# Performance work log

Measured on AMD Instinct MI355X. Metric: run time of the kernel, lower is better.

## Reference

```python
import jax, jax.numpy as jnp
import numpy as np

D_MODEL = 1024
H = 16
T = 1024
B = 8

def setup_inputs() -> dict:
    key = jax.random.key(0)
    k0, k1, k2, k3, k4 = jax.random.split(key, 5)
    return {
        "x": jax.random.normal(k0, (B, T, D_MODEL), dtype=jnp.float32),
        "Wq": jax.random.normal(k1, (D_MODEL, D_MODEL), dtype=jnp.float32),
        "Wk": jax.random.normal(k2, (D_MODEL, D_MODEL), dtype=jnp.float32),
        "Wv": jax.random.normal(k3, (D_MODEL, D_MODEL), dtype=jnp.float32),
        "Wp": jax.random.normal(k4, (D_MODEL, D_MODEL), dtype=jnp.float32),
    }

def reference(x, Wq, Wk, Wv, Wp):
    b, t, d = x.shape
    dh = d // H
    # projections
    q = (x @ Wq).reshape(b, t, H, dh)
    k = (x @ Wk).reshape(b, t, H, dh)
    v = (x @ Wv).reshape(b, t, H, dh)
    # [b, h, t, t] attention scores, scaled by sqrt(d_head)
    scores = jnp.einsum("bqhd,bkhd->bhqk", q, k) / jnp.sqrt(jnp.float32(dh))
    attn = jax.nn.softmax(scores, axis=-1)
    # [b, h, t, dh] -> [b, t, d]
    out = jnp.einsum("bhqk,bkhd->bqhd", attn, v).reshape(b, t, d)
    return out @ Wp
```

## Files before the change

### kernel.cpp

```cpp
#include <hip/hip_runtime.h>
#include <math.h>


typedef unsigned short u16;
typedef unsigned int u32;
typedef __bf16  bf16x8 __attribute__((ext_vector_type(8)));
typedef unsigned short u16x8 __attribute__((ext_vector_type(8)));
typedef unsigned short u16x4 __attribute__((ext_vector_type(4)));
typedef short s16x4 __attribute__((ext_vector_type(4)));
typedef unsigned int u32x2 __attribute__((ext_vector_type(2)));
typedef float f32x4 __attribute__((ext_vector_type(4)));

#define MFMA16(a,b,c) __builtin_amdgcn_mfma_f32_16x16x32_bf16((a),(b),(c),0,0,0)
#define MFMA16K16(a,b,c) __builtin_amdgcn_mfma_f32_16x16x16bf16_1k((a),(b),(c),0,0,0)

static __device__ __forceinline__ u16 f2b(float f){
  unsigned u = __builtin_bit_cast(unsigned, f);
  u += 0x7fffu + ((u >> 16) & 1u);
  return (u16)(u >> 16);
}
static __device__ __forceinline__ float b2f(u16 h){
  unsigned u = ((unsigned)h) << 16;
  return __builtin_bit_cast(float, u);
}
static __device__ __forceinline__ bf16x8 ldsfrag(const u16* p){
  return __builtin_bit_cast(bf16x8, *(const u16x8*)p);
}
static __device__ __forceinline__ u32 packhi(float fa, float fb){
  return __builtin_amdgcn_perm(__builtin_bit_cast(u32, fa),
                               __builtin_bit_cast(u32, fb), 0x07060302u);
}
static __device__ __forceinline__ void gld16(const void* g, void* l){
  __builtin_amdgcn_global_load_lds(
      (const __attribute__((address_space(1))) void*)g,
      (__attribute__((address_space(3))) void*)l, 16, 0, 0);
}


__global__ __launch_bounds__(256) void split_x_kernel(
    const float* __restrict__ x, u16* __restrict__ xh, u16* __restrict__ xl, int n)
{
  int i = (blockIdx.x * 256 + threadIdx.x) * 8;
  if (i >= n) return;
  float4 v0 = *(const float4*)(x + i);
  float4 v1 = *(const float4*)(x + i + 4);
  float vv[8] = {v0.x, v0.y, v0.z, v0.w, v1.x, v1.y, v1.z, v1.w};
  u16x8 hv, lv;
#pragma unroll
  for (int j = 0; j < 8; j++){
    u16 hb = f2b(vv[j]);
    hv[j] = hb;
    lv[j] = f2b(vv[j] - b2f(hb));
  }
  *(u16x8*)(xh + i) = hv;
  *(u16x8*)(xl + i) = lv;
}

__global__ __launch_bounds__(256) void transpose4_kernel(
    const float* __restrict__ Wq, const float* __restrict__ Wk,
    const float* __restrict__ Wv, const float* __restrict__ Wp,
    u16* __restrict__ qh_, u16* __restrict__ ql_,
    u16* __restrict__ kh_, u16* __restrict__ kl_,
    u16* __restrict__ vt_, u16* __restrict__ pt_)
{
  __shared__ float t[32][33];
  const int z = blockIdx.z;
  const float* W = (z == 0) ? Wq : (z == 1) ? Wk : (z == 2) ? Wv : Wp;
  u16* Th = (z == 0) ? qh_ : (z == 1) ? kh_ : (z == 2) ? vt_ : pt_;
  u16* Tl = (z == 0) ? ql_ : (z == 1) ? kl_ : nullptr;
  int n0 = blockIdx.x * 32, k0 = blockIdx.y * 32;
  int tx = threadIdx.x, ty = threadIdx.y;
#pragma unroll
  for (int i = 0; i < 4; i++){
    int k = k0 + ty + i * 8;
    t[ty + i * 8][tx] = W[(size_t)k * 1024 + n0 + tx];
  }
  __syncthreads();
#pragma unroll
  for (int i = 0; i < 4; i++){
    int n = n0 + ty + i * 8;
    float v = t[tx][ty + i * 8];
    u16 h = f2b(v);
    Th[(size_t)n * 1024 + k0 + tx] = h;
    if (Tl) Tl[(size_t)n * 1024 + k0 + tx] = f2b(v - b2f(h));
  }
}

template<int OUTMODE>
__global__ __launch_bounds__(256) void gemm_bt_kernel(
    const u16* __restrict__ A, const u16* __restrict__ Bt, void* __restrict__ Cv,
    int M, int N, int K)
{
  __shared__ __attribute__((aligned(16))) u16 lA[4096], lB[4096];
  const int tid = threadIdx.x, lane = tid & 63, wave = tid >> 6;
  const int quad = lane >> 4, l15 = lane & 15;
  const int row0 = blockIdx.x * 128, col0 = blockIdx.y * 128;
  const int wm = wave >> 1, wn = wave & 1;
  const int sr = lane >> 2, sc = (lane & 3) * 8;
  f32x4 acc[4][4];
#pragma unroll
  for (int mt = 0; mt < 4; mt++)
#pragma unroll
    for (int nt = 0; nt < 4; nt++) acc[mt][nt] = (f32x4)0.0f;

  for (int k0 = 0; k0 < K; k0 += 32){
#pragma unroll
    for (int i = 0; i < 2; i++){
      int c = wave * 2 + i;
      gld16(A  + (size_t)(row0 + c * 16 + sr) * K + k0 + sc, &lA[c * 512]);
      gld16(Bt + (size_t)(col0 + c * 16 + sr) * K + k0 + sc, &lB[c * 512]);
    }
    __syncthreads();
    bf16x8 a[4], b[4];
#pragma unroll
    for (int t = 0; t < 4; t++){
      a[t] = ldsfrag(&lA[(wm * 64 + t * 16 + l15) * 32 + quad * 8]);
      b[t] = ldsfrag(&lB[(wn * 64 + t * 16 + l15) * 32 + quad * 8]);
    }
#pragma unroll
    for (int mt = 0; mt < 4; mt++)
#pragma unroll
      for (int nt = 0; nt < 4; nt++)
        acc[mt][nt] = MFMA16(a[mt], b[nt], acc[mt][nt]);
    __syncthreads();
  }
  if (OUTMODE == 2){
#pragma unroll
    for (int mt = 0; mt < 4; mt++)
#pragma unroll
      for (int nt = 0; nt < 4; nt++){
        int row = row0 + wm * 64 + mt * 16 + quad * 4;
        int col = col0 + wn * 64 + nt * 16 + l15;
        int bb = row >> 10, tt = row & 1023;
        int hh = (col >> 6) & 15, d = col & 63;
        int bhI = bb * 16 + hh;
        int ktile = tt >> 7, fkt = (tt >> 4) & 7, qF = (tt >> 2) & 3;
        int nd = d >> 4, l15F = d & 15;
        size_t idx = ((((size_t)(bhI * 8 + ktile) * 8 + fkt) * 4 + nd) * 64
                      + qF * 16 + l15F) * 4;
        u16x4 vals;
#pragma unroll
        for (int r = 0; r < 4; r++) vals[r] = f2b(acc[mt][nt][r]);
        *(u16x4*)(((u16*)Cv) + idx) = vals;
      }
  } else {
#pragma unroll
    for (int mt = 0; mt < 4; mt++)
#pragma unroll
      for (int nt = 0; nt < 4; nt++)
#pragma unroll
        for (int r = 0; r < 4; r++){
          int row = row0 + wm * 64 + mt * 16 + quad * 4 + r;
          int col = col0 + wn * 64 + nt * 16 + l15;
          ((float*)Cv)[(size_t)row * N + col] = acc[mt][nt][r];
        }
  }
}

__global__ __launch_bounds__(512, 2) void gemm_qk_kernel(
    const u16* __restrict__ Ah, const u16* __restrict__ Al,
    const u16* __restrict__ Bh, const u16* __restrict__ Bl,
    u16* __restrict__ Qhf, u16* __restrict__ Qlf,
    u16* __restrict__ Khf, u16* __restrict__ Klf, int M, int N, int K)
{
  __shared__ __attribute__((aligned(16))) u16 sA[2][2][8192], sB[2][2][8192];
  const int tid = threadIdx.x, lane = tid & 63, wave = tid >> 6;
  const int quad = lane >> 4, l15 = lane & 15;
  const int wm = wave >> 2, wn = wave & 3;
  const int row0 = blockIdx.x * 256, col0 = blockIdx.y * 256;
  const int f0a = (wave & 3) | ((wave & 4) << 1);
  const int f0b = (wave & 1) | ((wave >> 1) << 2);
  const size_t fstride = (size_t)16 * K;
  const size_t abase = (size_t)(row0 + l15) * K + quad * 8;
  const size_t bbase = (size_t)(col0 + l15) * K + quad * 8;
  (void)M; (void)N;

  f32x4 acc[8][4];
#pragma unroll
  for (int mt = 0; mt < 8; mt++)
#pragma unroll
    for (int nt = 0; nt < 4; nt++) acc[mt][nt] = (f32x4)0.0f;

#define STAGE_ALL(KK, NB) do {                                                           \
    gld16(Ah + abase + (size_t)f0a * fstride + (KK), &sA[NB][0][f0a * 512]);             \
    gld16(Al + abase + (size_t)f0a * fstride + (KK), &sA[NB][1][f0a * 512]);             \
    gld16(Bh + bbase + (size_t)f0b * fstride + (KK), &sB[NB][0][f0b * 512]);             \
    gld16(Bl + bbase + (size_t)f0b * fstride + (KK), &sB[NB][1][f0b * 512]);             \
    gld16(Bh + bbase + (size_t)(f0b + 2) * fstride + (KK), &sB[NB][0][(f0b + 2) * 512]); \
    gld16(Bl + bbase + (size_t)(f0b + 2) * fstride + (KK), &sB[NB][1][(f0b + 2) * 512]); \
    gld16(Ah + abase + (size_t)(f0a + 4) * fstride + (KK), &sA[NB][0][(f0a + 4) * 512]); \
    gld16(Al + abase + (size_t)(f0a + 4) * fstride + (KK), &sA[NB][1][(f0a + 4) * 512]); \
  } while (0)
#define RD_A2(DH, DL, B4, I0, BUF) do {                           \
    _Pragma("unroll")                                             \
    for (int i = (I0); i < (I0) + 2; i++){                        \
      int fa = wm * 8 + (B4) + i;                                 \
      DH[i] = ldsfrag(&sA[BUF][0][fa * 512 + lane * 8]);          \
      DL[i] = ldsfrag(&sA[BUF][1][fa * 512 + lane * 8]);          \
    } } while (0)
#define RD_B2(DH, DL, B2, BUF) do {                               \
    _Pragma("unroll")                                             \
    for (int j = 0; j < 2; j++){                                  \
      int fb = wn * 4 + (B2) + j;                                 \
      DH[j] = ldsfrag(&sB[BUF][0][fb * 512 + lane * 8]);          \
      DL[j] = ldsfrag(&sB[BUF][1][fb * 512 + lane * 8]);          \
    } } while (0)
#define MM(AH, AL, BH, BL, M0, N0) do {                                      \
    __builtin_amdgcn_s_setprio(1);                                           \
    _Pragma("unroll")                                                        \
    for (int i = 0; i < 4; i++)                                              \
      _Pragma("unroll")                                                      \
      for (int j = 0; j < 2; j++){                                           \
        acc[(M0) + i][(N0) + j] = MFMA16(AL[i], BH[j], acc[(M0) + i][(N0) + j]); \
        acc[(M0) + i][(N0) + j] = MFMA16(AH[i], BL[j], acc[(M0) + i][(N0) + j]); \
        acc[(M0) + i][(N0) + j] = MFMA16(AH[i], BH[j], acc[(M0) + i][(N0) + j]); \
      }                                                                      \
    __builtin_amdgcn_s_setprio(0);                                           \
  } while (0)

  const int NT = K >> 5;
  STAGE_ALL(0, 0);

  bf16x8 a0h[4], a0l[4], a1h[4], a1l[4];
  bf16x8 b0h[2], b0l[2], b1h[2], b1l[2];
#pragma unroll 2
  for (int t = 0; t < NT; t++){
    const int buf = t & 1, nb = buf ^ 1;
    const int kn = ((t + 1) & (NT - 1)) * 32;
    asm volatile("s_waitcnt vmcnt(0)" ::: "memory");
    asm volatile("s_barrier" ::: "memory");
    STAGE_ALL(kn, nb);
    RD_A2(a0h, a0l, 0, 0, buf);
    RD_A2(a0h, a0l, 0, 2, buf);
    RD_B2(b0h, b0l, 0, buf);
    RD_B2(b1h, b1l, 2, buf);
    MM(a0h, a0l, b0h, b0l, 0, 0);
    RD_A2(a1h, a1l, 4, 0, buf);
    MM(a0h, a0l, b1h, b1l, 0, 2);
    RD_A2(a1h, a1l, 4, 2, buf);
    RD_B2(b0h, b0l, 0, buf);
    MM(a1h, a1l, b1h, b1l, 4, 2);
    MM(a1h, a1l, b0h, b0l, 4, 0);
  }
  asm volatile("s_waitcnt vmcnt(0)" ::: "memory");

#undef STAGE_ALL
#undef RD_A2
#undef RD_B2
#undef MM

  const bool isQ = (col0 < 1024);
#pragma unroll
  for (int mt = 0; mt < 8; mt++)
#pragma unroll
    for (int nt = 0; nt < 4; nt++)
#pragma unroll
      for (int r = 0; r < 4; r++){
        int row = row0 + wm * 128 + mt * 16 + quad * 4 + r;
        int col = col0 + wn * 64 + nt * 16 + l15;
        int bb = row >> 10, tt = row & 1023;
        int hh = (col >> 6) & 15, d = col & 63;
        int bhI = bb * 16 + hh;
        int kc = d >> 5, qF = (d >> 3) & 3, j = d & 7;
        float v = acc[mt][nt][r];
        u16 hi = f2b(v);
        u16 lo = f2b(v - b2f(hi));
        if (isQ){
          int qtile = tt >> 7, rr = tt & 127;
          int wv = rr >> 5, mtF = (rr >> 4) & 1, l15F = tt & 15;
          size_t idx = ((((size_t)(bhI * 8 + qtile) * 4 + wv) * 2 + mtF) * 2 + kc) * 512
                       + (qF * 16 + l15F) * 8 + j;
          Qhf[idx] = hi; Qlf[idx] = lo;
        } else {
          int ktile = tt >> 7, fkt = (tt >> 4) & 7, l15F = tt & 15;
          size_t idx = (((size_t)(bhI * 8 + ktile) * 8 + fkt) * 2 + kc) * 512
                       + (qF * 16 + l15F) * 8 + j;
          Khf[idx] = hi; Klf[idx] = lo;
        }
      }
}

__global__ __launch_bounds__(256, 3) void attn_kernel(
    const u16* __restrict__ Qhf, const u16* __restrict__ Qlf,
    const u16* __restrict__ Khf, const u16* __restrict__ Klf,
    const u16* __restrict__ Vf, u16* __restrict__ O)
{
  __shared__ __attribute__((aligned(16))) u16 lKh[2][4096], lKl[2][4096], lV[2][4096];
  const int tid = threadIdx.x, lane = tid & 63, wave = tid >> 6;
  const int quad = lane >> 4, l15 = lane & 15;
  const int qt = blockIdx.x >> 7, bh = blockIdx.x & 127;
  const int b = bh >> 4, h = bh & 15;
  const int q0 = qt * 128;
  const float BETA = 0.18033688011112042f;

  bf16x8 qh[2][2], ql[2][2];
  {
    size_t qbase = (size_t)(bh * 8 + qt) * 8192 + wave * 2048 + lane * 8;
    u16* sh = &lKh[0][0];  u16* sl = &lKl[0][0];
#pragma unroll
    for (int i = 0; i < 4; i++){
      gld16(Qhf + qbase + i * 512, sh + wave * 2048 + i * 512);
      gld16(Qlf + qbase + i * 512, sl + wave * 2048 + i * 512);
    }
    __syncthreads();
#pragma unroll
    for (int mt = 0; mt < 2; mt++)
#pragma unroll
      for (int kc = 0; kc < 2; kc++){
        int off = wave * 2048 + (mt * 2 + kc) * 512 + lane * 8;
        qh[mt][kc] = ldsfrag(sh + off);
        ql[mt][kc] = ldsfrag(sl + off);
      }
    __syncthreads();
  }

  float m_i[2] = {-3.0e38f, -3.0e38f}, l_i[2] = {0.0f, 0.0f};
  f32x4 o_acc[2][4];
#pragma unroll
  for (int mt = 0; mt < 2; mt++)
#pragma unroll
    for (int nd = 0; nd < 4; nd++) o_acc[mt][nd] = (f32x4)0.0f;

  const size_t pan = (size_t)bh * 65536;
#pragma unroll
  for (int i = 0; i < 2; i++){
    int c = wave * 2 + i;
    gld16(Khf + pan + c * 512 + lane * 8, &lKh[0][c * 512]);
    gld16(Klf + pan + c * 512 + lane * 8, &lKl[0][c * 512]);
    gld16(Vf  + pan + c * 512 + lane * 8, &lV [0][c * 512]);
  }

#pragma unroll 1
  for (int j = 0; j < 16; j++){
    const int cur = j & 1;
    __syncthreads();
    if (j < 15){
      size_t nb = pan + (size_t)(j + 1) * 4096;
      const int nxt = cur ^ 1;
#pragma unroll
      for (int i = 0; i < 2; i++){
        int c = wave * 2 + i;
        gld16(Khf + nb + c * 512 + lane * 8, &lKh[nxt][c * 512]);
        gld16(Klf + nb + c * 512 + lane * 8, &lKl[nxt][c * 512]);
        gld16(Vf  + nb + c * 512 + lane * 8, &lV [nxt][c * 512]);
      }
    }

    f32x4 s[2][4];
#pragma unroll
    for (int qt2 = 0; qt2 < 2; qt2++)
#pragma unroll
      for (int f4 = 0; f4 < 4; f4++) s[qt2][f4] = (f32x4)0.0f;
#pragma unroll
    for (int f4 = 0; f4 < 4; f4++){
      int aoff = f4 * 1024 + lane * 8;
      bf16x8 kh0 = ldsfrag(&lKh[cur][aoff]);
      bf16x8 kh1 = ldsfrag(&lKh[cur][aoff + 512]);
      bf16x8 kl0 = ldsfrag(&lKl[cur][aoff]);
      bf16x8 kl1 = ldsfrag(&lKl[cur][aoff + 512]);
#pragma unroll
      for (int qt2 = 0; qt2 < 2; qt2++){
        s[qt2][f4] = MFMA16(kl0, qh[qt2][0], s[qt2][f4]);
        s[qt2][f4] = MFMA16(kl1, qh[qt2][1], s[qt2][f4]);
        s[qt2][f4] = MFMA16(kh0, ql[qt2][0], s[qt2][f4]);
        s[qt2][f4] = MFMA16(kh1, ql[qt2][1], s[qt2][f4]);
        s[qt2][f4] = MFMA16(kh0, qh[qt2][0], s[qt2][f4]);
        s[qt2][f4] = MFMA16(kh1, qh[qt2][1], s[qt2][f4]);
      }
    }

    float alpha[2];
#pragma unroll
    for (int qt2 = 0; qt2 < 2; qt2++){
      f32x4 mv = s[qt2][0];
#pragma unroll
      for (int f4 = 1; f4 < 4; f4++){
        mv[0] = fmaxf(mv[0], s[qt2][f4][0]); mv[1] = fmaxf(mv[1], s[qt2][f4][1]);
        mv[2] = fmaxf(mv[2], s[qt2][f4][2]); mv[3] = fmaxf(mv[3], s[qt2][f4][3]);
      }
      float mx = fmaxf(fmaxf(mv[0], mv[1]), fmaxf(mv[2], mv[3]));
      mx = fmaxf(mx, __shfl_xor(mx, 16));
      mx = fmaxf(mx, __shfl_xor(mx, 32));
      float mn = fmaxf(m_i[qt2], mx);
      alpha[qt2] = __builtin_amdgcn_exp2f((m_i[qt2] - mn) * BETA);
      m_i[qt2] = mn;
      float mb = mn * BETA;
      f32x4 ps = (f32x4)0.0f;
#pragma unroll
      for (int f4 = 0; f4 < 4; f4++)
#pragma unroll
        for (int r = 0; r < 4; r++){
          float p = __builtin_amdgcn_exp2f(s[qt2][f4][r] * BETA - mb);
          s[qt2][f4][r] = p;
          ps[r] += p;
        }
      float rs = (ps[0] + ps[1]) + (ps[2] + ps[3]);
      rs += __shfl_xor(rs, 16);
      rs += __shfl_xor(rs, 32);
      l_i[qt2] = l_i[qt2] * alpha[qt2] + rs;
    }

#pragma unroll
    for (int mt = 0; mt < 2; mt++)
#pragma unroll
      for (int r = 0; r < 4; r++){
        float ar = __shfl(alpha[mt], quad * 4 + r);
#pragma unroll
        for (int nd = 0; nd < 4; nd++) o_acc[mt][nd][r] *= ar;
      }

#pragma unroll
    for (int f4 = 0; f4 < 4; f4++){
      s16x4 vb[4];
#pragma unroll
      for (int nd = 0; nd < 4; nd++)
        vb[nd] = __builtin_bit_cast(s16x4,
                   *(const u16x4*)&lV[cur][(f4 * 4 + nd) * 256 + lane * 4]);
#pragma unroll
      for (int qt2 = 0; qt2 < 2; qt2++){
        u32x2 pd;
        pd[0] = packhi(s[qt2][f4][1], s[qt2][f4][0]);
        pd[1] = packhi(s[qt2][f4][3], s[qt2][f4][2]);
        s16x4 pa = __builtin_bit_cast(s16x4, pd);
#pragma unroll
        for (int nd = 0; nd < 4; nd++)
          o_acc[qt2][nd] = MFMA16K16(pa, vb[nd], o_acc[qt2][nd]);
      }
    }
  }

#pragma unroll
  for (int mt = 0; mt < 2; mt++)
#pragma unroll
    for (int r = 0; r < 4; r++){
      float lr = __shfl(l_i[mt], quad * 4 + r);
      float inv = 1.0f / lr;
      int t = q0 + wave * 32 + mt * 16 + quad * 4 + r;
      size_t rowoff = (size_t)(b * 1024 + t) * 1024 + h * 64;
#pragma unroll
      for (int nd = 0; nd < 4; nd++)
        O[rowoff + nd * 16 + l15] = f2b(o_acc[mt][nd][r] * inv);
    }
}

extern "C" void kernel_launch(void* const* d_in, const int* in_sizes, int n_in,
                              void* d_out, int out_size, void* d_ws, size_t ws_size,
                              hipStream_t stream)
{
  const float* x  = (const float*)d_in[0];
  const float* Wq = (const float*)d_in[1];
  const float* Wk = (const float*)d_in[2];
  const float* Wv = (const float*)d_in[3];
  const float* Wp = (const float*)d_in[4];
  float* out = (float*)d_out;
  char* ws = (char*)d_ws;
  const size_t MB = 1024 * 1024;
  u16* xh   = (u16*)(ws + 0);
  u16* xl   = (u16*)(ws + 16 * MB);
  u16* wqkh = (u16*)(ws + 32 * MB);
  u16* wqkl = (u16*)(ws + 36 * MB);
  u16* wvt  = (u16*)(ws + 40 * MB);
  u16* wpt  = (u16*)(ws + 42 * MB);
  u16* Qhf  = (u16*)(ws + 44 * MB);
  u16* Qlf  = (u16*)(ws + 60 * MB);
  u16* Khf  = (u16*)(ws + 76 * MB);
  u16* Klf  = (u16*)(ws + 92 * MB);
  u16* Vf   = (u16*)(ws + 108 * MB);
  u16* obuf = xh;
  (void)in_sizes; (void)n_in; (void)out_size; (void)ws_size;

  split_x_kernel<<<4096, 256, 0, stream>>>(x, xh, xl, 8 * 1024 * 1024);
  transpose4_kernel<<<dim3(32, 32, 4), dim3(32, 8), 0, stream>>>(
      Wq, Wk, Wv, Wp, wqkh, wqkl, wqkh + 1024 * 1024, wqkl + 1024 * 1024, wvt, wpt);
  gemm_qk_kernel<<<dim3(32, 8), 512, 0, stream>>>(xh, xl, wqkh, wqkl,
                                                  Qhf, Qlf, Khf, Klf, 8192, 2048, 1024);
  gemm_bt_kernel<2><<<dim3(64, 8), 256, 0, stream>>>(xh, wvt, (void*)Vf, 8192, 1024, 1024);
  attn_kernel<<<1024, 256, 0, stream>>>(Qhf, Qlf, Khf, Klf, Vf, obuf);
  gemm_bt_kernel<0><<<dim3(64, 8), 256, 0, stream>>>(obuf, wpt, (void*)out, 8192, 1024, 1024);
}
```

Before: 350.7 us.

## Interleave global-to-LDS staging with MFMA phases using extra barriers in QKV GEMM

Splits the per-iteration global-to-LDS prefetch into three groups and issues each between LDS fragment reads and MFMA blocks, with s_barrier after each group. The aim is to spread memory traffic across the compute phases and keep waves in lockstep, in the style of ping-pong scheduling. In exchange it adds four barriers per iteration, which can stall waves if they are not balanced.

```diff
diff --git a/kernel.cpp b/kernel.cpp
--- a/kernel.cpp
+++ b/kernel.cpp
@@ -181,13 +181,17 @@
 #pragma unroll
     for (int nt = 0; nt < 4; nt++) acc[mt][nt] = (f32x4)0.0f;
 
-#define STAGE_ALL(KK, NB) do {                                                           \
-    gld16(Ah + abase + (size_t)f0a * fstride + (KK), &sA[NB][0][f0a * 512]);             \
-    gld16(Al + abase + (size_t)f0a * fstride + (KK), &sA[NB][1][f0a * 512]);             \
-    gld16(Bh + bbase + (size_t)f0b * fstride + (KK), &sB[NB][0][f0b * 512]);             \
-    gld16(Bl + bbase + (size_t)f0b * fstride + (KK), &sB[NB][1][f0b * 512]);             \
+#define STAGE_G0(KK, NB) do {                                              \
+    gld16(Ah + abase + (size_t)f0a * fstride + (KK), &sA[NB][0][f0a * 512]); \
+    gld16(Al + abase + (size_t)f0a * fstride + (KK), &sA[NB][1][f0a * 512]); \
+    gld16(Bh + bbase + (size_t)f0b * fstride + (KK), &sB[NB][0][f0b * 512]); \
+    gld16(Bl + bbase + (size_t)f0b * fstride + (KK), &sB[NB][1][f0b * 512]); \
+  } while (0)
+#define STAGE_G1(KK, NB) do {                                                        \
     gld16(Bh + bbase + (size_t)(f0b + 2) * fstride + (KK), &sB[NB][0][(f0b + 2) * 512]); \
     gld16(Bl + bbase + (size_t)(f0b + 2) * fstride + (KK), &sB[NB][1][(f0b + 2) * 512]); \
+  } while (0)
+#define STAGE_G2(KK, NB) do {                                                        \
     gld16(Ah + abase + (size_t)(f0a + 4) * fstride + (KK), &sA[NB][0][(f0a + 4) * 512]); \
     gld16(Al + abase + (size_t)(f0a + 4) * fstride + (KK), &sA[NB][1][(f0a + 4) * 512]); \
   } while (0)
@@ -217,9 +221,13 @@
       }                                                                      \
     __builtin_amdgcn_s_setprio(0);                                           \
   } while (0)
+#define VMCNT0() asm volatile("s_waitcnt vmcnt(0)" ::: "memory")
+#define BARRIER() asm volatile("s_barrier" ::: "memory")
 
   const int NT = K >> 5;
-  STAGE_ALL(0, 0);
+  STAGE_G0(0, 0);
+  STAGE_G1(0, 0);
+  STAGE_G2(0, 0);
 
   bf16x8 a0h[4], a0l[4], a1h[4], a1l[4];
   bf16x8 b0h[2], b0l[2], b1h[2], b1l[2];
@@ -227,27 +235,37 @@
   for (int t = 0; t < NT; t++){
     const int buf = t & 1, nb = buf ^ 1;
     const int kn = ((t + 1) & (NT - 1)) * 32;
-    asm volatile("s_waitcnt vmcnt(0)" ::: "memory");
-    asm volatile("s_barrier" ::: "memory");
-    STAGE_ALL(kn, nb);
+    VMCNT0();
+    BARRIER();
     RD_A2(a0h, a0l, 0, 0, buf);
     RD_A2(a0h, a0l, 0, 2, buf);
     RD_B2(b0h, b0l, 0, buf);
+    STAGE_G0(kn, nb);
+    BARRIER();
+    MM(a0h, a0l, b0h, b0l, 0, 0);
     RD_B2(b1h, b1l, 2, buf);
-    MM(a0h, a0l, b0h, b0l, 0, 0);
+    STAGE_G1(kn, nb);
+    BARRIER();
+    MM(a0h, a0l, b1h, b1l, 0, 2);
     RD_A2(a1h, a1l, 4, 0, buf);
-    MM(a0h, a0l, b1h, b1l, 0, 2);
     RD_A2(a1h, a1l, 4, 2, buf);
+    STAGE_G2(kn, nb);
+    BARRIER();
+    MM(a1h, a1l, b1h, b1l, 4, 2);
     RD_B2(b0h, b0l, 0, buf);
-    MM(a1h, a1l, b1h, b1l, 4, 2);
+    BARRIER();
     MM(a1h, a1l, b0h, b0l, 4, 0);
   }
-  asm volatile("s_waitcnt vmcnt(0)" ::: "memory");
-
-#undef STAGE_ALL
+  VMCNT0();
+
+#undef STAGE_G0
+#undef STAGE_G1
+#undef STAGE_G2
 #undef RD_A2
 #undef RD_B2
 #undef MM
+#undef VMCNT0
+#undef BARRIER
 
   const bool isQ = (col0 < 1024);
 #pragma unroll
```

After: 340.0 us. 1.03x faster.
